# Performance work log

Measured on AMD Instinct MI355X. Metric: run time of the kernel, lower is better.

Reference implementation:

```python
import jax, jax.numpy as jnp
import numpy as np

B, S, D, H = 2, 4096, 1024, 16
DH = D // H            # head dim = 64
W = 256                # one-sided attention window (attention_window // 2)
NC = S // W            # number of query chunks
NEG = -1e9


def setup_inputs() -> dict:
    key = jax.random.key(0)
    ks = jax.random.split(key, 8)
    sc = 0.02
    return {
        "hidden_states": jax.random.normal(ks[0], (B, S, D), jnp.float32),
        # additive float mask: 0 = local token, <0 = padding, >0 = global. All zeros here.
        "attention_mask": jnp.zeros((B, 1, 1, S), jnp.float32),
        "Wq": jax.random.normal(ks[1], (D, D), jnp.float32) * sc,
        "bq": jnp.zeros((D,), jnp.float32),
        "Wk": jax.random.normal(ks[2], (D, D), jnp.float32) * sc,
        "bk": jnp.zeros((D,), jnp.float32),
        "Wv": jax.random.normal(ks[3], (D, D), jnp.float32) * sc,
        "bv": jnp.zeros((D,), jnp.float32),
        "Wo": jax.random.normal(ks[4], (D, D), jnp.float32) * sc,
        "bo": jnp.zeros((D,), jnp.float32),
    }


def _heads(x, w, b):
    # [B,S,D] -> [B,H,S,DH]
    return (x @ w + b).reshape(B, S, H, DH).transpose(0, 2, 1, 3)


def _forward(hidden_states, attention_mask, Wq, bq, Wk, bk, Wv, bv, Wo, bo):
    mask = attention_mask[:, 0, 0, :]                    # [B,S] additive key mask
    q = _heads(hidden_states, Wq, bq) / jnp.sqrt(jnp.float32(DH))
    k = _heads(hidden_states, Wk, bk)
    v = _heads(hidden_states, Wv, bv)

    # Overlapping key/value chunks: chunk c covers padded positions [c*W, c*W+3W),
    # i.e. global keys [c*W - W, c*W + 2W) -- the union of the windows of its W queries.
    idx = jnp.arange(NC)[:, None] * W + jnp.arange(3 * W)[None, :]   # [NC,3W] into padded axis
    k_pad = jnp.pad(k, ((0, 0), (0, 0), (W, W), (0, 0)))
    v_pad = jnp.pad(v, ((0, 0), (0, 0), (W, W), (0, 0)))
    k_ch = k_pad[:, :, idx]                               # [B,H,NC,3W,DH]
    v_ch = v_pad[:, :, idx]                               # [B,H,NC,3W,DH]
    mask_ch = jnp.pad(mask, ((0, 0), (W, W)))[:, idx]     # [B,NC,3W]

    q_ch = q.reshape(B, H, NC, W, DH)
    scores = jnp.einsum('bhcqd,bhckd->bhcqk', q_ch, k_ch)  # [B,H,NC,W,3W]

    # Band mask: query local p attends key local o with 0 <= o - p <= 2W.
    rel = jnp.arange(3 * W)[None, :] - jnp.arange(W)[:, None]        # [W,3W]
    band = (rel >= 0) & (rel <= 2 * W)
    key_gidx = idx - W                                               # global key index
    valid = (key_gidx >= 0) & (key_gidx < S)                         # [NC,3W]
    allowed = band[None, :, :] & valid[:, None, :]                   # [NC,W,3W]

    scores = scores + mask_ch[:, None, :, None, :]
    scores = jnp.where(allowed[None, None], scores, NEG)
    probs = jax.nn.softmax(scores, axis=-1)

    out = jnp.einsum('bhcqk,bhckd->bhcqd', probs, v_ch)    # [B,H,NC,W,DH]
    out = out.reshape(B, H, S, DH).transpose(0, 2, 1, 3).reshape(B, S, D)
    return out @ Wo + bo


def reference(hidden_states, attention_mask, Wq, bq, Wk, bk, Wv, bv, Wo, bo):
    return _forward(hidden_states, attention_mask, Wq, bq, Wk, bk, Wv, bv, Wo, bo)
```

## Files before the change

### kernel.cpp

```cpp
#include <hip/hip_runtime.h>

typedef unsigned short u16;
typedef __bf16 bf16x8 __attribute__((ext_vector_type(8)));
typedef u16 u16x8 __attribute__((ext_vector_type(8)));
typedef float f32x4 __attribute__((ext_vector_type(4)));
typedef unsigned uint2v __attribute__((ext_vector_type(2)));

#define LOG2E 1.4426950408889634f

static __device__ __forceinline__ u16 f2bf(float f) {
    union { float f; unsigned u; } x; x.f = f;
    unsigned r = x.u + 0x7fffu + ((x.u >> 16) & 1u);
    return (u16)(r >> 16);
}

static __device__ __forceinline__ unsigned cvtpk(float lo, float hi) {
    unsigned r;
    asm("v_cvt_pk_bf16_f32 %0, %1, %2" : "=v"(r) : "v"(lo), "v"(hi));
    return r;
}

static __device__ __forceinline__ void gl_lds16(const void* g, void* l) {
    __builtin_amdgcn_global_load_lds(
        (const __attribute__((address_space(1))) void*)g,
        (__attribute__((address_space(3))) void*)l, 16, 0, 0);
}

__global__ __launch_bounds__(256) void cvt_k(const float* __restrict__ src,
                                             u16* __restrict__ dst, int n) {
    int i = (blockIdx.x * 256 + threadIdx.x) * 4;
    if (i < n) {
        float4 v = *(const float4*)(src + i);
        ushort4 o;
        o.x = f2bf(v.x); o.y = f2bf(v.y); o.z = f2bf(v.z); o.w = f2bf(v.w);
        *(ushort4*)(dst + i) = o;
    }
}

__global__ __launch_bounds__(256) void transw_k(const float* __restrict__ w0,
                                                const float* __restrict__ w1,
                                                const float* __restrict__ w2,
                                                const float* __restrict__ w3,
                                                u16* __restrict__ wt) {
    __shared__ float T[64][65];
    const float* src = (blockIdx.z == 0) ? w0 : (blockIdx.z == 1) ? w1
                     : (blockIdx.z == 2) ? w2 : w3;
    u16* dst = wt + (size_t)blockIdx.z * 1048576;
    const int k0 = blockIdx.x * 64, n0 = blockIdx.y * 64;
    const int rr = threadIdx.x >> 6, col = threadIdx.x & 63;
#pragma unroll
    for (int i = 0; i < 16; ++i) {
        int row = i * 4 + rr;
        T[row][col] = src[(size_t)(k0 + row) * 1024 + n0 + col];
    }
    __syncthreads();
#pragma unroll
    for (int i = 0; i < 16; ++i) {
        int row = i * 4 + rr;
        dst[(size_t)(n0 + row) * 1024 + k0 + col] = f2bf(T[col][row]);
    }
}

__global__ __launch_bounds__(256, 2) void gemm_k(
    const u16* __restrict__ A, const u16* __restrict__ WT0,
    const float* __restrict__ b0, const float* __restrict__ b1,
    const float* __restrict__ b2,
    u16* __restrict__ o0, u16* __restrict__ o1, u16* __restrict__ o2,
    float* __restrict__ oF, int mode) {
    __shared__ alignas(16) u16 Al[128 * 32];
    __shared__ alignas(16) u16 Bl[128 * 32];

    const int tid = threadIdx.x;
    const int lane = tid & 63;
    const int wv = tid >> 6;
    const int wr = wv >> 1, wc = wv & 1;
    const int l15 = lane & 15, l4 = lane >> 4;

    const int mbase = blockIdx.x * 128;
    const int sel = blockIdx.y >> 3;
    const int nb = (blockIdx.y & 7) * 128;

    const u16* Ab = A + (size_t)mbase * 1024;
    const u16* Bb = WT0 + (size_t)sel * 1048576 + (size_t)nb * 1024;

    const int srow = tid >> 2;
    const int scol = (tid & 3) * 8;

    f32x4 acc[4][4] = {};

    for (int k0 = 0; k0 < 1024; k0 += 32) {
        char* la = (char*)Al + wv * 1024;
        char* lb = (char*)Bl + wv * 1024;
        gl_lds16(Ab + (size_t)srow * 1024 + k0 + scol, la);
        gl_lds16(Ab + (size_t)(srow + 64) * 1024 + k0 + scol, la + 4096);
        gl_lds16(Bb + (size_t)srow * 1024 + k0 + scol, lb);
        gl_lds16(Bb + (size_t)(srow + 64) * 1024 + k0 + scol, lb + 4096);
        __syncthreads();

        bf16x8 af[4], bfr[4];
#pragma unroll
        for (int mr = 0; mr < 4; ++mr)
            af[mr] = *(const bf16x8*)(Al + (wr * 64 + mr * 16 + l15) * 32 + l4 * 8);
#pragma unroll
        for (int nr = 0; nr < 4; ++nr)
            bfr[nr] = *(const bf16x8*)(Bl + (wc * 64 + nr * 16 + l15) * 32 + l4 * 8);
#pragma unroll
        for (int mr = 0; mr < 4; ++mr)
#pragma unroll
            for (int nr = 0; nr < 4; ++nr)
                acc[mr][nr] = __builtin_amdgcn_mfma_f32_16x16x32_bf16(
                    af[mr], bfr[nr], acc[mr][nr], 0, 0, 0);
        __syncthreads();
    }

    const float* bias = (sel == 0) ? b0 : ((sel == 1) ? b1 : b2);
    u16* oH = (sel == 0) ? o0 : ((sel == 1) ? o1 : o2);
    const float scale = (mode == 0 && sel == 0) ? 0.125f * LOG2E : 1.0f;

#pragma unroll
    for (int mr = 0; mr < 4; ++mr)
#pragma unroll
        for (int nr = 0; nr < 4; ++nr) {
            int col = nb + wc * 64 + nr * 16 + l15;
            float bv_ = bias[col];
#pragma unroll
            for (int j = 0; j < 4; ++j) {
                int row = mbase + wr * 64 + mr * 16 + l4 * 4 + j;
                float v = (acc[mr][nr][j] + bv_) * scale;
                if (mode == 0) {
                    int b_ = row >> 12, s_ = row & 4095;
                    int h_ = col >> 6, d_ = col & 63;
                    oH[(((size_t)(b_ * 16 + h_) * 4096) + s_) * 64 + d_] = f2bf(v);
                } else {
                    oF[(size_t)row * 1024 + col] = v;
                }
            }
        }
}

__global__ __launch_bounds__(256, 3) void attn_k(
    const u16* __restrict__ Qh, const u16* __restrict__ Kh,
    const u16* __restrict__ Vh, const float* __restrict__ mask,
    u16* __restrict__ attnb) {
    __shared__ alignas(16) u16 Kt[2][4096];
    __shared__ alignas(16) u16 Vt[2][4096];
    __shared__ alignas(16) u16 Pl[4][1024];

    const int tid = threadIdx.x;
    const int lane = tid & 63;
    const int wv = tid >> 6;
    const int hw = blockIdx.x;
    const int lg = (hw & 7) * 128 + (hw >> 3);
    const int c = lg & 31;
    const int h = (lg >> 5) & 15;
    const int b = lg >> 9;

    const size_t bh = (size_t)(b * 16 + h) * 4096;
    const u16* Qb = Qh + bh * 64;
    const u16* Kb = Kh + bh * 64;
    const u16* Vb = Vh + bh * 64;
    const float* mb = mask + b * 4096;

    const int l15 = lane & 15;
    const int l4 = lane >> 4;
    const int qbase = c * 128 + wv * 32;
    const int gkbase = c * 128 - 256;

    bf16x8 qf[2][2];
#pragma unroll
    for (int qt = 0; qt < 2; ++qt)
#pragma unroll
        for (int kc = 0; kc < 2; ++kc)
            qf[qt][kc] = *(const bf16x8*)(Qb + (size_t)(qbase + qt * 16 + l15) * 64 + kc * 32 + l4 * 8);

    f32x4 Ov[4][2] = {};
    float lsum[2] = {0.f, 0.f};
    float m = -3.0e38f;

    const int kslot = lane & 7;
    const int krow8 = lane >> 3;
    const int vrow = tid >> 3;
    const int vd0 = (tid & 7) * 8;

    const int tmin = wv >> 1;
    const int tmax_t = 8 + (wv >> 1);

    {
#pragma unroll
        for (int i = 0; i < 2; ++i) {
            int row = i * 32 + wv * 8 + krow8;
            int key = min(max(gkbase + row, 0), 4095);
            gl_lds16(Kb + (size_t)key * 64 + ((kslot ^ (row & 7)) * 8),
                     &Kt[0][(i * 32 + wv * 8) * 64]);
        }
#pragma unroll
        for (int i = 0; i < 2; ++i) {
            int vk = i * 32 + vrow;
            int key = min(max(gkbase + vk, 0), 4095);
            u16x8 vv = *(const u16x8*)(Vb + (size_t)key * 64 + vd0);
            int vbx = (vk >> 3) ^ (tid & 7);
#pragma unroll
            for (int e = 0; e < 8; ++e)
                Vt[0][(vd0 + e) * 64 + ((vbx ^ e) * 8) + (vk & 7)] = vv[e];
        }
    }
    __syncthreads();

    for (int t = 0; t < 10; ++t) {
        const int cur = t & 1, nxt = cur ^ 1;
        const int gk0 = gkbase + t * 64;
        const bool pre = (t < 9);

        u16x8 vv[2] = {};
        if (pre) {
            const int gk0n = gk0 + 64;
#pragma unroll
            for (int i = 0; i < 2; ++i) {
                int row = i * 32 + wv * 8 + krow8;
                int key = min(max(gk0n + row, 0), 4095);
                gl_lds16(Kb + (size_t)key * 64 + ((kslot ^ (row & 7)) * 8),
                         &Kt[nxt][(i * 32 + wv * 8) * 64]);
            }
#pragma unroll
            for (int i = 0; i < 2; ++i) {
                int key = min(max(gk0n + i * 32 + vrow, 0), 4095);
                vv[i] = *(const u16x8*)(Vb + (size_t)key * 64 + vd0);
            }
        }

        if (t >= tmin && t <= tmax_t) {
            f32x4 mv[4];
#pragma unroll
            for (int kb = 0; kb < 4; ++kb) {
                int idx = min(max(gk0 + kb * 16 + l4 * 4, 0), 4092);
                mv[kb] = *(const f32x4*)(mb + idx);
            }

            f32x4 sc[4][2] = {};
            __builtin_amdgcn_s_setprio(1);
#pragma unroll
            for (int kc = 0; kc < 2; ++kc)
#pragma unroll
                for (int kb = 0; kb < 4; ++kb) {
                    int r = kb * 16 + l15;
                    bf16x8 kf = *(const bf16x8*)(&Kt[cur][r * 64 + (((kc * 4 + l4) ^ (r & 7)) * 8)]);
                    sc[kb][0] = __builtin_amdgcn_mfma_f32_16x16x32_bf16(kf, qf[0][kc], sc[kb][0], 0, 0, 0);
                    sc[kb][1] = __builtin_amdgcn_mfma_f32_16x16x32_bf16(kf, qf[1][kc], sc[kb][1], 0, 0, 0);
                }
            __builtin_amdgcn_s_setprio(0);

            float tmx = -3.0e9f;
            const int kb0 = gk0 + l4 * 4;
            const int ub0 = kb0 - (qbase + l15) + 256;
#pragma unroll
            for (int kb = 0; kb < 4; ++kb)
#pragma unroll
                for (int qt = 0; qt < 2; ++qt)
#pragma unroll
                    for (int j = 0; j < 4; ++j) {
                        float sv = fmaf(mv[kb][j], LOG2E, sc[kb][qt][j]);
                        unsigned band = (unsigned)(ub0 + kb * 16 + j - qt * 16);
                        unsigned keyv = (unsigned)(kb0 + kb * 16 + j);
                        bool ok = (band <= 512u) && (keyv < 4096u);
                        sv = ok ? sv : -3.0e9f;
                        sc[kb][qt][j] = sv;
                        tmx = fmaxf(tmx, sv);
                    }
            tmx = fmaxf(tmx, __shfl_xor(tmx, 1));
            tmx = fmaxf(tmx, __shfl_xor(tmx, 2));
            tmx = fmaxf(tmx, __shfl_xor(tmx, 4));
            tmx = fmaxf(tmx, __shfl_xor(tmx, 8));
            tmx = fmaxf(tmx, __shfl_xor(tmx, 16));
            tmx = fmaxf(tmx, __shfl_xor(tmx, 32));

            if (tmx > m) {
                float alpha = exp2f(m - tmx);
                m = tmx;
#pragma unroll
                for (int nd = 0; nd < 4; ++nd)
#pragma unroll
                    for (int qt = 0; qt < 2; ++qt) Ov[nd][qt] *= alpha;
                lsum[0] *= alpha;
                lsum[1] *= alpha;
            }

#pragma unroll
            for (int kb = 0; kb < 4; ++kb)
#pragma unroll
                for (int qt = 0; qt < 2; ++qt) {
                    float s0 = 0.f;
#pragma unroll
                    for (int j = 0; j < 4; ++j) {
                        float p = exp2f(sc[kb][qt][j] - m);
                        sc[kb][qt][j] = p;
                        s0 += p;
                    }
                    lsum[qt] += s0;
                }

            u16* Pw = &Pl[wv][0];
            const int prow = l15 * 64;
#pragma unroll
            for (int qt = 0; qt < 2; ++qt) {
#pragma unroll
                for (int kb = 0; kb < 4; ++kb) {
                    uint2v pk;
                    pk[0] = cvtpk(sc[kb][qt][0], sc[kb][qt][1]);
                    pk[1] = cvtpk(sc[kb][qt][2], sc[kb][qt][3]);
                    int g = (((kb * 2 + (l4 >> 1)) ^ (l15 & 7)) * 8) + (l4 & 1) * 4;
                    *(uint2v*)(Pw + prow + g) = pk;
                }
#pragma unroll
                for (int kc = 0; kc < 2; ++kc) {
                    bf16x8 pf = *(const bf16x8*)(Pw + prow + (((kc * 4 + l4) ^ (l15 & 7)) * 8));
                    __builtin_amdgcn_s_setprio(1);
#pragma unroll
                    for (int nd = 0; nd < 4; ++nd) {
                        int r2 = nd * 16 + l15;
                        bf16x8 vf = *(const bf16x8*)(&Vt[cur][r2 * 64 +
                            (((kc * 4 + l4) ^ (r2 & 7) ^ ((r2 >> 3) & 7)) * 8)]);
                        Ov[nd][qt] = __builtin_amdgcn_mfma_f32_16x16x32_bf16(vf, pf, Ov[nd][qt], 0, 0, 0);
                    }
                    __builtin_amdgcn_s_setprio(0);
                }
            }
        }

        if (pre) {
#pragma unroll
            for (int i = 0; i < 2; ++i) {
                int vk = i * 32 + vrow;
                int vbx = (vk >> 3) ^ (tid & 7);
#pragma unroll
                for (int e = 0; e < 8; ++e)
                    Vt[nxt][(vd0 + e) * 64 + ((vbx ^ e) * 8) + (vk & 7)] = vv[i][e];
            }
        }
        __syncthreads();
    }

    lsum[0] += __shfl_xor(lsum[0], 16);
    lsum[0] += __shfl_xor(lsum[0], 32);
    lsum[1] += __shfl_xor(lsum[1], 16);
    lsum[1] += __shfl_xor(lsum[1], 32);
    float inv0 = 1.0f / lsum[0];
    float inv1 = 1.0f / lsum[1];
#pragma unroll
    for (int qt = 0; qt < 2; ++qt) {
        float inv = qt ? inv1 : inv0;
        size_t rowb = ((size_t)b * 4096 + qbase + qt * 16 + l15) * 1024 + h * 64 + l4 * 4;
#pragma unroll
        for (int nd = 0; nd < 4; ++nd) {
            uint2v o;
            o[0] = cvtpk(Ov[nd][qt][0] * inv, Ov[nd][qt][1] * inv);
            o[1] = cvtpk(Ov[nd][qt][2] * inv, Ov[nd][qt][3] * inv);
            *(uint2v*)(&attnb[rowb + nd * 16]) = o;
        }
    }
}

extern "C" void kernel_launch(void* const* d_in, const int* in_sizes, int n_in,
                              void* d_out, int out_size, void* d_ws, size_t ws_size,
                              hipStream_t stream) {
    (void)in_sizes; (void)n_in; (void)out_size; (void)ws_size;
    const float* hid  = (const float*)d_in[0];
    const float* mask = (const float*)d_in[1];
    const float* Wq = (const float*)d_in[2];
    const float* bq = (const float*)d_in[3];
    const float* Wk = (const float*)d_in[4];
    const float* bk = (const float*)d_in[5];
    const float* Wv = (const float*)d_in[6];
    const float* bv = (const float*)d_in[7];
    const float* Wo = (const float*)d_in[8];
    const float* bo = (const float*)d_in[9];
    float* out = (float*)d_out;

    char* ws = (char*)d_ws;
    u16* hidb  = (u16*)(ws);
    u16* wt    = (u16*)(ws + (16u << 20));
    u16* Qh    = (u16*)(ws + (24u << 20));
    u16* Kh    = (u16*)(ws + (40u << 20));
    u16* Vh    = (u16*)(ws + (56u << 20));
    u16* attnb = (u16*)(ws + (72u << 20));

    cvt_k<<<dim3(8192), dim3(256), 0, stream>>>(hid, hidb, 8388608);
    transw_k<<<dim3(16, 16, 4), dim3(256), 0, stream>>>(Wq, Wk, Wv, Wo, wt);
    gemm_k<<<dim3(64, 24), dim3(256), 0, stream>>>(hidb, wt, bq, bk, bv,
                                                   Qh, Kh, Vh, (float*)nullptr, 0);
    attn_k<<<dim3(1024), dim3(256), 0, stream>>>(Qh, Kh, Vh, mask, attnb);
    gemm_k<<<dim3(64, 8), dim3(256), 0, stream>>>(attnb, wt + 3 * 1048576, bo, bo, bo,
                                                  (u16*)nullptr, (u16*)nullptr, (u16*)nullptr,
                                                  out, 1);
}
```

Before: 195.4 us.

## Stage mask in LDS, skip band checks on interior tiles, lazy softmax rescale

Preloads the scaled key mask for the block's key span into shared memory once, instead of issuing global loads every tile. Adds a fast path that skips the per-element band and bounds checks when a tile lies fully inside the window. Replaces the per-tile max reduction and rescale with a wave vote that only reduces and rescales when the new max exceeds the running max by more than 8 (log2 units). Also fuses the exp/sum with the bf16 packing and stages the output through LDS so global stores are full 16-byte row writes. The lazy rescale lets probabilities exceed 1 by up to 2^8 before renormalization, which risks bf16 precision, and the LDS output staging reuses Kt after the final barrier.

```diff
diff --git a/kernel.cpp b/kernel.cpp
--- a/kernel.cpp
+++ b/kernel.cpp
@@ -145,6 +145,7 @@
     __shared__ alignas(16) u16 Kt[2][4096];
     __shared__ alignas(16) u16 Vt[2][4096];
     __shared__ alignas(16) u16 Pl[4][1024];
+    __shared__ float maskl[640];
 
     const int tid = threadIdx.x;
     const int lane = tid & 63;
@@ -181,9 +182,10 @@
     const int krow8 = lane >> 3;
     const int vrow = tid >> 3;
     const int vd0 = (tid & 7) * 8;
+    const int vbx = (vrow >> 3) ^ (tid & 7);
 
     const int tmin = wv >> 1;
-    const int tmax_t = 8 + (wv >> 1);
+    const int tmaxw = 8 + (wv >> 1);
 
     {
 #pragma unroll
@@ -198,10 +200,14 @@
             int vk = i * 32 + vrow;
             int key = min(max(gkbase + vk, 0), 4095);
             u16x8 vv = *(const u16x8*)(Vb + (size_t)key * 64 + vd0);
-            int vbx = (vk >> 3) ^ (tid & 7);
+            int bx = ((vk >> 3) ^ (tid & 7));
 #pragma unroll
             for (int e = 0; e < 8; ++e)
-                Vt[0][(vd0 + e) * 64 + ((vbx ^ e) * 8) + (vk & 7)] = vv[e];
+                Vt[0][(vd0 + e) * 64 + ((bx ^ e) * 8) + (vk & 7)] = vv[e];
+        }
+        for (int i = tid; i < 640; i += 256) {
+            int gm = gkbase + i;
+            maskl[i] = (gm >= 0 && gm < 4096) ? mb[gm] * LOG2E : 0.f;
         }
     }
     __syncthreads();
@@ -228,14 +234,7 @@
             }
         }
 
-        if (t >= tmin && t <= tmax_t) {
-            f32x4 mv[4];
-#pragma unroll
-            for (int kb = 0; kb < 4; ++kb) {
-                int idx = min(max(gk0 + kb * 16 + l4 * 4, 0), 4092);
-                mv[kb] = *(const f32x4*)(mb + idx);
-            }
-
+        if (t >= tmin && t <= tmaxw) {
             f32x4 sc[4][2] = {};
             __builtin_amdgcn_s_setprio(1);
 #pragma unroll
@@ -249,33 +248,54 @@
                 }
             __builtin_amdgcn_s_setprio(0);
 
+            f32x4 mv[4];
+#pragma unroll
+            for (int kb = 0; kb < 4; ++kb)
+                mv[kb] = *(const f32x4*)(maskl + t * 64 + kb * 16 + l4 * 4);
+
+            const int dkq = gk0 - qbase;
+            const bool full = (dkq >= -225) && (dkq <= 193) && (gk0 >= 0) && (gk0 <= 4032);
             float tmx = -3.0e9f;
-            const int kb0 = gk0 + l4 * 4;
-            const int ub0 = kb0 - (qbase + l15) + 256;
-#pragma unroll
-            for (int kb = 0; kb < 4; ++kb)
-#pragma unroll
-                for (int qt = 0; qt < 2; ++qt)
-#pragma unroll
-                    for (int j = 0; j < 4; ++j) {
-                        float sv = fmaf(mv[kb][j], LOG2E, sc[kb][qt][j]);
-                        unsigned band = (unsigned)(ub0 + kb * 16 + j - qt * 16);
-                        unsigned keyv = (unsigned)(kb0 + kb * 16 + j);
-                        bool ok = (band <= 512u) && (keyv < 4096u);
-                        sv = ok ? sv : -3.0e9f;
-                        sc[kb][qt][j] = sv;
-                        tmx = fmaxf(tmx, sv);
-                    }
-            tmx = fmaxf(tmx, __shfl_xor(tmx, 1));
-            tmx = fmaxf(tmx, __shfl_xor(tmx, 2));
-            tmx = fmaxf(tmx, __shfl_xor(tmx, 4));
-            tmx = fmaxf(tmx, __shfl_xor(tmx, 8));
-            tmx = fmaxf(tmx, __shfl_xor(tmx, 16));
-            tmx = fmaxf(tmx, __shfl_xor(tmx, 32));
-
-            if (tmx > m) {
-                float alpha = exp2f(m - tmx);
-                m = tmx;
+            if (full) {
+#pragma unroll
+                for (int kb = 0; kb < 4; ++kb)
+#pragma unroll
+                    for (int qt = 0; qt < 2; ++qt)
+#pragma unroll
+                        for (int j = 0; j < 4; ++j) {
+                            float sv = sc[kb][qt][j] + mv[kb][j];
+                            sc[kb][qt][j] = sv;
+                            tmx = fmaxf(tmx, sv);
+                        }
+            } else {
+                const int kq0 = gk0 + l4 * 4 - (qbase + l15) + 256;
+                const int kv0 = gk0 + l4 * 4;
+#pragma unroll
+                for (int kb = 0; kb < 4; ++kb)
+#pragma unroll
+                    for (int qt = 0; qt < 2; ++qt)
+#pragma unroll
+                        for (int j = 0; j < 4; ++j) {
+                            float sv = sc[kb][qt][j] + mv[kb][j];
+                            unsigned band = (unsigned)(kq0 + kb * 16 + j - qt * 16);
+                            unsigned keyv = (unsigned)(kv0 + kb * 16 + j);
+                            bool ok = (band <= 512u) && (keyv < 4096u);
+                            sv = ok ? sv : -3.0e9f;
+                            sc[kb][qt][j] = sv;
+                            tmx = fmaxf(tmx, sv);
+                        }
+            }
+
+            if (!__all(tmx <= m + 8.0f)) {
+                float tr = tmx;
+                tr = fmaxf(tr, __shfl_xor(tr, 1));
+                tr = fmaxf(tr, __shfl_xor(tr, 2));
+                tr = fmaxf(tr, __shfl_xor(tr, 4));
+                tr = fmaxf(tr, __shfl_xor(tr, 8));
+                tr = fmaxf(tr, __shfl_xor(tr, 16));
+                tr = fmaxf(tr, __shfl_xor(tr, 32));
+                float alpha = exp2f(m - tr);
+                m = tr;
 #pragma unroll
                 for (int nd = 0; nd < 4; ++nd)
 #pragma unroll
@@ -284,32 +304,25 @@
                 lsum[1] *= alpha;
             }
 
-#pragma unroll
-            for (int kb = 0; kb < 4; ++kb)
-#pragma unroll
-                for (int qt = 0; qt < 2; ++qt) {
-                    float s0 = 0.f;
-#pragma unroll
-                    for (int j = 0; j < 4; ++j) {
-                        float p = exp2f(sc[kb][qt][j] - m);
-                        sc[kb][qt][j] = p;
-                        s0 += p;
-                    }
-                    lsum[qt] += s0;
-                }
-
             u16* Pw = &Pl[wv][0];
             const int prow = l15 * 64;
 #pragma unroll
             for (int qt = 0; qt < 2; ++qt) {
+                float s0 = 0.f;
 #pragma unroll
                 for (int kb = 0; kb < 4; ++kb) {
+                    float p0 = exp2f(sc[kb][qt][0] - m);
+                    float p1 = exp2f(sc[kb][qt][1] - m);
+                    float p2 = exp2f(sc[kb][qt][2] - m);
+                    float p3 = exp2f(sc[kb][qt][3] - m);
+                    s0 += (p0 + p1) + (p2 + p3);
                     uint2v pk;
-                    pk[0] = cvtpk(sc[kb][qt][0], sc[kb][qt][1]);
-                    pk[1] = cvtpk(sc[kb][qt][2], sc[kb][qt][3]);
+                    pk[0] = cvtpk(p0, p1);
+                    pk[1] = cvtpk(p2, p3);
                     int g = (((kb * 2 + (l4 >> 1)) ^ (l15 & 7)) * 8) + (l4 & 1) * 4;
                     *(uint2v*)(Pw + prow + g) = pk;
                 }
+                lsum[qt] += s0;
 #pragma unroll
                 for (int kc = 0; kc < 2; ++kc) {
                     bf16x8 pf = *(const bf16x8*)(Pw + prow + (((kc * 4 + l4) ^ (l15 & 7)) * 8));
@@ -330,10 +343,10 @@
 #pragma unroll
             for (int i = 0; i < 2; ++i) {
                 int vk = i * 32 + vrow;
-                int vbx = (vk >> 3) ^ (tid & 7);
+                int bx = ((vk >> 3) ^ (tid & 7));
 #pragma unroll
                 for (int e = 0; e < 8; ++e)
-                    Vt[nxt][(vd0 + e) * 64 + ((vbx ^ e) * 8) + (vk & 7)] = vv[i][e];
+                    Vt[nxt][(vd0 + e) * 64 + ((bx ^ e) * 8) + (vk & 7)] = vv[i][e];
             }
         }
         __syncthreads();
@@ -345,17 +358,27 @@
     lsum[1] += __shfl_xor(lsum[1], 32);
     float inv0 = 1.0f / lsum[0];
     float inv1 = 1.0f / lsum[1];
+
+    u16* Ob = &Kt[0][0] + wv * 2048;
 #pragma unroll
     for (int qt = 0; qt < 2; ++qt) {
         float inv = qt ? inv1 : inv0;
-        size_t rowb = ((size_t)b * 4096 + qbase + qt * 16 + l15) * 1024 + h * 64 + l4 * 4;
+        int row = qt * 16 + l15;
 #pragma unroll
         for (int nd = 0; nd < 4; ++nd) {
-            uint2v o;
-            o[0] = cvtpk(Ov[nd][qt][0] * inv, Ov[nd][qt][1] * inv);
-            o[1] = cvtpk(Ov[nd][qt][2] * inv, Ov[nd][qt][3] * inv);
-            *(uint2v*)(&attnb[rowb + nd * 16]) = o;
-        }
+            uint2v pk;
+            pk[0] = cvtpk(Ov[nd][qt][0] * inv, Ov[nd][qt][1] * inv);
+            pk[1] = cvtpk(Ov[nd][qt][2] * inv, Ov[nd][qt][3] * inv);
+            int g = nd * 2 + (l4 >> 1);
+            *(uint2v*)((char*)Ob + row * 128 + ((g ^ (row & 7)) * 16) + (l4 & 1) * 8) = pk;
+        }
+    }
+#pragma unroll
+    for (int i = 0; i < 4; ++i) {
+        int row = i * 8 + (lane >> 3);
+        int g = lane & 7;
+        u16x8 ov = *(const u16x8*)((char*)Ob + row * 128 + ((g ^ (row & 7)) * 16));
+        *(u16x8*)(&attnb[((size_t)b * 4096 + c * 128 + wv * 32 + row) * 1024 + h * 64 + g * 8]) = ov;
     }
 }
 
```

Result: slower. 227.5 us (+16.4%).

## Single-buffer V tile, stage mask in LDS, per-row softmax max for occupancy

Applied to the files above, without the earlier changes.

The V tile drops from double to single buffering, with an extra barrier before it is overwritten, so LDS use shrinks and launch bounds go from 3 to 4 blocks per CU. The additive mask is pre-scaled by log2(e) and loaded once per block into LDS instead of being read from global memory on every tile. The online softmax now keeps a running max per query tile and reduces it across only the 16-lane row groups, replacing the wavefront-wide max and conditional rescale. The costs are an extra __syncthreads per iteration and loss of overlap for the V writes, traded for higher occupancy and fewer shuffles.

```diff
diff --git a/kernel.cpp b/kernel.cpp
--- a/kernel.cpp
+++ b/kernel.cpp
@@ -138,13 +138,14 @@
         }
 }
 
-__global__ __launch_bounds__(256, 3) void attn_k(
+__global__ __launch_bounds__(256, 4) void attn_k(
     const u16* __restrict__ Qh, const u16* __restrict__ Kh,
     const u16* __restrict__ Vh, const float* __restrict__ mask,
     u16* __restrict__ attnb) {
     __shared__ alignas(16) u16 Kt[2][4096];
-    __shared__ alignas(16) u16 Vt[2][4096];
+    __shared__ alignas(16) u16 Vt[4096];
     __shared__ alignas(16) u16 Pl[4][1024];
+    __shared__ alignas(16) float maskl[640];
 
     const int tid = threadIdx.x;
     const int lane = tid & 63;
@@ -175,7 +176,7 @@
 
     f32x4 Ov[4][2] = {};
     float lsum[2] = {0.f, 0.f};
-    float m = -3.0e38f;
+    float m[2] = {-3.0e38f, -3.0e38f};
 
     const int kslot = lane & 7;
     const int krow8 = lane >> 3;
@@ -201,7 +202,11 @@
             int vbx = (vk >> 3) ^ (tid & 7);
 #pragma unroll
             for (int e = 0; e < 8; ++e)
-                Vt[0][(vd0 + e) * 64 + ((vbx ^ e) * 8) + (vk & 7)] = vv[e];
+                Vt[(vd0 + e) * 64 + ((vbx ^ e) * 8) + (vk & 7)] = vv[e];
+        }
+        for (int i = tid; i < 640; i += 256) {
+            int gm = gkbase + i;
+            maskl[i] = (gm >= 0 && gm < 4096) ? mb[gm] * LOG2E : 0.f;
         }
     }
     __syncthreads();
@@ -231,10 +236,8 @@
         if (t >= tmin && t <= tmax_t) {
             f32x4 mv[4];
 #pragma unroll
-            for (int kb = 0; kb < 4; ++kb) {
-                int idx = min(max(gk0 + kb * 16 + l4 * 4, 0), 4092);
-                mv[kb] = *(const f32x4*)(mb + idx);
-            }
+            for (int kb = 0; kb < 4; ++kb)
+                mv[kb] = *(const f32x4*)(maskl + t * 64 + kb * 16 + l4 * 4);
 
             f32x4 sc[4][2] = {};
             __builtin_amdgcn_s_setprio(1);
@@ -249,7 +252,6 @@
                 }
             __builtin_amdgcn_s_setprio(0);
 
-            float tmx = -3.0e9f;
             const int kb0 = gk0 + l4 * 4;
             const int ub0 = kb0 - (qbase + l15) + 256;
 #pragma unroll
@@ -258,58 +260,47 @@
                 for (int qt = 0; qt < 2; ++qt)
 #pragma unroll
                     for (int j = 0; j < 4; ++j) {
-                        float sv = fmaf(mv[kb][j], LOG2E, sc[kb][qt][j]);
+                        float sv = sc[kb][qt][j] + mv[kb][j];
                         unsigned band = (unsigned)(ub0 + kb * 16 + j - qt * 16);
                         unsigned keyv = (unsigned)(kb0 + kb * 16 + j);
                         bool ok = (band <= 512u) && (keyv < 4096u);
-                        sv = ok ? sv : -3.0e9f;
-                        sc[kb][qt][j] = sv;
-                        tmx = fmaxf(tmx, sv);
+                        sc[kb][qt][j] = ok ? sv : -3.0e9f;
                     }
-            tmx = fmaxf(tmx, __shfl_xor(tmx, 1));
-            tmx = fmaxf(tmx, __shfl_xor(tmx, 2));
-            tmx = fmaxf(tmx, __shfl_xor(tmx, 4));
-            tmx = fmaxf(tmx, __shfl_xor(tmx, 8));
-            tmx = fmaxf(tmx, __shfl_xor(tmx, 16));
-            tmx = fmaxf(tmx, __shfl_xor(tmx, 32));
-
-            if (tmx > m) {
-                float alpha = exp2f(m - tmx);
-                m = tmx;
-#pragma unroll
-                for (int nd = 0; nd < 4; ++nd)
-#pragma unroll
-                    for (int qt = 0; qt < 2; ++qt) Ov[nd][qt] *= alpha;
-                lsum[0] *= alpha;
-                lsum[1] *= alpha;
-            }
-
-#pragma unroll
-            for (int kb = 0; kb < 4; ++kb)
-#pragma unroll
-                for (int qt = 0; qt < 2; ++qt) {
-                    float s0 = 0.f;
-#pragma unroll
-                    for (int j = 0; j < 4; ++j) {
-                        float p = exp2f(sc[kb][qt][j] - m);
-                        sc[kb][qt][j] = p;
-                        s0 += p;
-                    }
-                    lsum[qt] += s0;
-                }
 
             u16* Pw = &Pl[wv][0];
             const int prow = l15 * 64;
 #pragma unroll
             for (int qt = 0; qt < 2; ++qt) {
+                float mx = sc[0][qt][0];
+#pragma unroll
+                for (int kb = 0; kb < 4; ++kb)
+#pragma unroll
+                    for (int j = 0; j < 4; ++j) mx = fmaxf(mx, sc[kb][qt][j]);
+                mx = fmaxf(mx, __shfl_xor(mx, 16));
+                mx = fmaxf(mx, __shfl_xor(mx, 32));
+                float mnew = fmaxf(m[qt], mx);
+                float alpha = exp2f(m[qt] - mnew);
+                m[qt] = mnew;
+                lsum[qt] *= alpha;
+#pragma unroll
+                for (int nd = 0; nd < 4; ++nd) Ov[nd][qt] *= alpha;
+
+                float s0 = 0.f;
 #pragma unroll
                 for (int kb = 0; kb < 4; ++kb) {
+                    float p0 = exp2f(sc[kb][qt][0] - mnew);
+                    float p1 = exp2f(sc[kb][qt][1] - mnew);
+                    float p2 = exp2f(sc[kb][qt][2] - mnew);
+                    float p3 = exp2f(sc[kb][qt][3] - mnew);
+                    s0 += (p0 + p1) + (p2 + p3);
                     uint2v pk;
-                    pk[0] = cvtpk(sc[kb][qt][0], sc[kb][qt][1]);
-                    pk[1] = cvtpk(sc[kb][qt][2], sc[kb][qt][3]);
+                    pk[0] = cvtpk(p0, p1);
+                    pk[1] = cvtpk(p2, p3);
                     int g = (((kb * 2 + (l4 >> 1)) ^ (l15 & 7)) * 8) + (l4 & 1) * 4;
                     *(uint2v*)(Pw + prow + g) = pk;
                 }
+                lsum[qt] += s0;
+
 #pragma unroll
                 for (int kc = 0; kc < 2; ++kc) {
                     bf16x8 pf = *(const bf16x8*)(Pw + prow + (((kc * 4 + l4) ^ (l15 & 7)) * 8));
@@ -317,7 +308,7 @@
 #pragma unroll
                     for (int nd = 0; nd < 4; ++nd) {
                         int r2 = nd * 16 + l15;
-                        bf16x8 vf = *(const bf16x8*)(&Vt[cur][r2 * 64 +
+                        bf16x8 vf = *(const bf16x8*)(&Vt[r2 * 64 +
                             (((kc * 4 + l4) ^ (r2 & 7) ^ ((r2 >> 3) & 7)) * 8)]);
                         Ov[nd][qt] = __builtin_amdgcn_mfma_f32_16x16x32_bf16(vf, pf, Ov[nd][qt], 0, 0, 0);
                     }
@@ -326,6 +317,7 @@
             }
         }
 
+        __syncthreads();
         if (pre) {
 #pragma unroll
             for (int i = 0; i < 2; ++i) {
@@ -333,7 +325,7 @@
                 int vbx = (vk >> 3) ^ (tid & 7);
 #pragma unroll
                 for (int e = 0; e < 8; ++e)
-                    Vt[nxt][(vd0 + e) * 64 + ((vbx ^ e) * 8) + (vk & 7)] = vv[i][e];
+                    Vt[(vd0 + e) * 64 + ((vbx ^ e) * 8) + (vk & 7)] = vv[i][e];
             }
         }
         __syncthreads();
```

After: 203.2 us. 4.0% more time.
